# Kernel optimization log

Hardware: AMD Instinct MI355X
Metric: run time of the kernel (lower is better)

Reference implementation:

```python
import jax, jax.numpy as jnp
import numpy as np
from jax import lax

NPOINT = 2048
NSAMPLE = 32
RADIUS = 0.2


def setup_inputs() -> dict:
    key = jax.random.key(0)
    ks = jax.random.split(key, 6)
    B, N, C = 4, 16384, 64
    xyz = jax.random.normal(ks[0], (B, N, 3), jnp.float32)
    features = jax.random.normal(ks[1], (B, C, N), jnp.float32)

    def w(k, o, i):
        return jax.random.normal(k, (o, i), jnp.float32) * (1.0 / np.sqrt(i))

    W1 = w(ks[2], 64, C + 3)
    b1 = jnp.zeros((64,), jnp.float32)
    W2 = w(ks[3], 64, 64)
    b2 = jnp.zeros((64,), jnp.float32)
    W3 = w(ks[4], 128, 64)
    b3 = jnp.zeros((128,), jnp.float32)
    return {"xyz": xyz, "features": features, "W1": W1, "b1": b1,
            "W2": W2, "b2": b2, "W3": W3, "b3": b3}


def _fps(xyz, npoint):
    # Iterative furthest point sampling. xyz: (B, N, 3) -> (B, npoint) int32.
    B, N, _ = xyz.shape

    def step(carry, _):
        dist, last = carry  # dist: (B, N) running min sq-dist to chosen set
        p = jnp.take_along_axis(xyz, last[:, None, None], axis=1)  # (B,1,3)
        d = jnp.sum((xyz - p) ** 2, axis=-1)                        # (B,N)
        dist = jnp.minimum(dist, d)
        nxt = jnp.argmax(dist, axis=-1).astype(jnp.int32)
        return (dist, nxt), nxt

    init = (jnp.full((B, N), 1e10, xyz.dtype), jnp.zeros((B,), jnp.int32))
    _, rest = lax.scan(step, init, None, length=npoint - 1)  # (npoint-1, B)
    idx = jnp.concatenate([jnp.zeros((1, B), jnp.int32), rest], axis=0)
    return idx.T  # (B, npoint)


def _ball_query(xyz, new_xyz):
    # For each centroid pick up to NSAMPLE points within RADIUS (first-found
    # semantics, matching the PointNet++ CUDA ball_query: pad with first hit).
    B, N, _ = xyz.shape
    d2 = jnp.sum((new_xyz[:, :, None, :] - xyz[:, None, :, :]) ** 2, axis=-1)  # (B,S,N)
    cand = jnp.where(d2 < RADIUS * RADIUS, jnp.arange(N, dtype=jnp.int32), N)
    neg_vals, _ = lax.top_k(-cand, NSAMPLE)  # smallest NSAMPLE indices, in order
    sel = -neg_vals                           # (B,S,NSAMPLE)
    first = sel[..., :1]
    sel = jnp.where(sel == N, first, sel)     # pad empties with first hit
    return jnp.where(sel == N, 0, sel)        # fully-empty balls -> index 0


def reference(xyz, features, W1, b1, W2, b2, W3, b3):
    new_xyz_idx = _fps(xyz, NPOINT)                              # (B, S)
    new_xyz = jnp.take_along_axis(xyz, new_xyz_idx[..., None], axis=1)  # (B,S,3)
    idx = _ball_query(xyz, new_xyz)                              # (B,S,ns)
    B, S, ns = idx.shape
    C = features.shape[1]
    # Gather + center neighbor xyz: (B, 3, S, ns)
    gx = jnp.take_along_axis(xyz, idx.reshape(B, S * ns, 1), axis=1)
    gx = gx.reshape(B, S, ns, 3) - new_xyz[:, :, None, :]
    gx = gx.transpose(0, 3, 1, 2)
    # Gather neighbor features: (B, C, S, ns)
    gf = jnp.take_along_axis(features, idx.reshape(B, 1, S * ns), axis=2)
    gf = gf.reshape(B, C, S, ns)
    x = jnp.concatenate([gx, gf], axis=1)  # (B, C+3, S, ns)
    # SharedMLP: 1x1 conv + ReLU stack
    for W, b in ((W1, b1), (W2, b2), (W3, b3)):
        x = jax.nn.relu(jnp.einsum('oi,bisn->bosn', W, x) + b[None, :, None, None])
    new_features = x.max(axis=-1)  # (B, 128, S)
    return new_xyz, new_xyz_idx, new_features, idx
```

## Files before the change

kernel.cpp:

```cpp
#include <hip/hip_runtime.h>
#include <cstdint>

#define BATCH   4
#define NPTS    16384
#define NCH     64
#define NPOINT  2048
#define NSAMP   32
#define NBUCK   (NPTS / 16)

#define OFF_XYZ  0
#define OFF_IDX1 (BATCH*NPOINT*3)
#define OFF_FEAT (OFF_IDX1 + BATCH*NPOINT)
#define OFF_IDX3 (OFF_FEAT + BATCH*128*NPOINT)


__device__ __forceinline__ float sqd_exact(float dx, float dy, float dz) {
    float a = __fmul_rn(dx, dx);
    float b = __fmul_rn(dy, dy);
    float c = __fmul_rn(dz, dz);
    return __fadd_rn(__fadd_rn(a, b), c);
}

__device__ __forceinline__ int part3(int v) {
    return (v & 1) | ((v & 2) << 2) | ((v & 4) << 4) | ((v & 8) << 6);
}

__device__ __forceinline__ unsigned long long wave_max_u64(unsigned hi, unsigned lo) {
#define STAGE(ctrl, rmask)                                                      \
    {                                                                           \
        unsigned ohi = (unsigned)__builtin_amdgcn_update_dpp(0, (int)hi, ctrl, rmask, 0xf, false); \
        unsigned olo = (unsigned)__builtin_amdgcn_update_dpp(0, (int)lo, ctrl, rmask, 0xf, false); \
        bool take = (ohi > hi) || ((ohi == hi) & (olo > lo));                   \
        hi = take ? ohi : hi;                                                   \
        lo = take ? olo : lo;                                                   \
    }
    STAGE(0x111, 0xf)
    STAGE(0x112, 0xf)
    STAGE(0x114, 0xf)
    STAGE(0x118, 0xf)
    STAGE(0x142, 0xa)
    STAGE(0x143, 0xc)
#undef STAGE
    unsigned rhi = (unsigned)__builtin_amdgcn_readlane((int)hi, 63);
    unsigned rlo = (unsigned)__builtin_amdgcn_readlane((int)lo, 63);
    return ((unsigned long long)rhi << 32) | rlo;
}

__global__ __launch_bounds__(1024)
void binsort_kernel(const float* __restrict__ xyz, float* __restrict__ out) {
    const int b = blockIdx.x, t = threadIdx.x, lane = t & 63, wv = t >> 6;
    float4* pts4 = (float4*)(out + OFF_FEAT) + (size_t)b * NPTS;
    const float* xb = xyz + (size_t)b * (NPTS * 3);

    __shared__ int hist[4096];
    __shared__ int wsum[16];
    for (int k = t; k < 4096; k += 1024) hist[k] = 0;
    __syncthreads();

    const int base = t << 4;
    float f[48];
    {
        const float4* v4 = (const float4*)(xb + (size_t)base * 3);
#pragma unroll
        for (int q = 0; q < 12; ++q) {
            float4 v = v4[q];
            f[4*q+0] = v.x; f[4*q+1] = v.y; f[4*q+2] = v.z; f[4*q+3] = v.w;
        }
    }
    int cells[16];
    const float sc = 16.0f / 9.0f;
#pragma unroll
    for (int j = 0; j < 16; ++j) {
        int qx = (int)fminf(fmaxf((f[3*j+0] + 4.5f) * sc, 0.0f), 15.0f);
        int qy = (int)fminf(fmaxf((f[3*j+1] + 4.5f) * sc, 0.0f), 15.0f);
        int qz = (int)fminf(fmaxf((f[3*j+2] + 4.5f) * sc, 0.0f), 15.0f);
        cells[j] = part3(qx) | (part3(qy) << 1) | (part3(qz) << 2);
        atomicAdd(&hist[cells[j]], 1);
    }
    __syncthreads();

    int h0 = hist[4*t], h1 = hist[4*t+1], h2 = hist[4*t+2], h3 = hist[4*t+3];
    int s = h0 + h1 + h2 + h3;
    int ps = s;
#pragma unroll
    for (int off = 1; off <= 32; off <<= 1) {
        int o = __shfl_up(ps, off, 64);
        if (lane >= off) ps += o;
    }
    if (lane == 63) wsum[wv] = ps;
    __syncthreads();
    int wbase = 0;
    for (int w = 0; w < wv; ++w) wbase += wsum[w];
    int excl = wbase + ps - s;
    hist[4*t]   = excl;
    hist[4*t+1] = excl + h0;
    hist[4*t+2] = excl + h0 + h1;
    hist[4*t+3] = excl + h0 + h1 + h2;
    __syncthreads();

#pragma unroll
    for (int j = 0; j < 16; ++j) {
        int pos = atomicAdd(&hist[cells[j]], 1);
        pts4[pos] = make_float4(f[3*j+0], f[3*j+1], f[3*j+2],
                                __int_as_float(base + j));
    }
}

__global__ __launch_bounds__(1024)
void fps_kernel(const float* __restrict__ xyz, float* __restrict__ out) {
    const int b = blockIdx.x, t = threadIdx.x, lane = t & 63;
    const float4* __restrict__ pts = (const float4*)(out + OFF_FEAT) + (size_t)b * NPTS;
    const float* __restrict__ xb = xyz + (size_t)b * (NPTS * 3);
    float* oxyz = out + OFF_XYZ  + (size_t)b * (NPOINT * 3);
    float* oidx = out + OFF_IDX1 + (size_t)b * NPOINT;

    __shared__ float s_dist[NPTS];
    __shared__ unsigned long long s_key[NBUCK];
    __shared__ int s_wl[NBUCK];
    __shared__ int s_cnt;
    __shared__ unsigned long long s_gkey;

    float bnx, bxx, bny, bxy, bnz, bxz;
    {
        float4 p0 = pts[t * 16];
        bnx = bxx = p0.x; bny = bxy = p0.y; bnz = bxz = p0.z;
#pragma unroll
        for (int j = 1; j < 16; ++j) {
            float4 p = pts[t * 16 + j];
            bnx = fminf(bnx, p.x); bxx = fmaxf(bxx, p.x);
            bny = fminf(bny, p.y); bxy = fmaxf(bxy, p.y);
            bnz = fminf(bnz, p.z); bxz = fmaxf(bxz, p.z);
        }
        float4 big = make_float4(1e10f, 1e10f, 1e10f, 1e10f);
#pragma unroll
        for (int k = 0; k < 4; ++k)
            *(float4*)&s_dist[t * 16 + k * 4] = big;
    }
    float maxdG = 1e10f;
    unsigned long long kv = 0;
    if (t == 0) { s_cnt = 0; s_gkey = 0ull; }

    float cx = xb[0], cy = xb[1], cz = xb[2];
    if (t == 0) { oxyz[0] = cx; oxyz[1] = cy; oxyz[2] = cz; oidx[0] = 0.0f; }
    __syncthreads();

    for (int it = 1; it < NPOINT; ++it) {
        float dxl = fmaxf(fmaxf(bnx - cx, cx - bxx), 0.0f);
        float dyl = fmaxf(fmaxf(bny - cy, cy - bxy), 0.0f);
        float dzl = fmaxf(fmaxf(bnz - cz, cz - bxz), 0.0f);
        float bb  = dxl * dxl + dyl * dyl + dzl * dzl;
        bool active = (bb * 0.99999f < maxdG);
        unsigned long long m = __ballot(active);
        int cntw = (int)__popcll(m);
        if (cntw) {
            int basep = 0;
            if (lane == 0) basep = atomicAdd(&s_cnt, cntw);
            basep = __shfl(basep, 0, 64);
            if (active) {
                int pos = basep + (int)__popcll(m & ((1ull << lane) - 1ull));
                s_wl[pos] = t;
            }
        }
        __syncthreads();
        if (t == 0) s_gkey = 0ull;
        const int K = s_cnt;
        const int sub = t & 3;
        for (int w = t >> 2; w < K; w += 256) {
            const int bid = s_wl[w];
            const int p0  = bid * 16 + sub * 4;
            float4 P0 = pts[p0 + 0], P1 = pts[p0 + 1],
                   P2 = pts[p0 + 2], P3 = pts[p0 + 3];
            float4 dv = *(float4*)&s_dist[p0];
            float mv = -1.0f; int bi = 0x7FFFFFFF;
#define UPD(P, DD)                                                              \
            {                                                                   \
                float d  = sqd_exact(__fsub_rn(P.x, cx),                        \
                                     __fsub_rn(P.y, cy),                        \
                                     __fsub_rn(P.z, cz));                       \
                float nd = fminf(DD, d);                                        \
                DD = nd;                                                        \
                int oi = __float_as_int(P.w);                                   \
                bool bet = (nd > mv) || ((nd == mv) & (oi < bi));               \
                mv = bet ? nd : mv;                                             \
                bi = bet ? oi : bi;                                             \
            }
            UPD(P0, dv.x) UPD(P1, dv.y) UPD(P2, dv.z) UPD(P3, dv.w)
#undef UPD
            *(float4*)&s_dist[p0] = dv;
#pragma unroll
            for (int off = 1; off <= 2; off <<= 1) {
                float omv = __shfl_xor(mv, off, 64);
                int   obi = __shfl_xor(bi, off, 64);
                bool take = (omv > mv) || ((omv == mv) & (obi < bi));
                mv = take ? omv : mv;
                bi = take ? obi : bi;
            }
            if (sub == 0)
                s_key[bid] = ((unsigned long long)__float_as_uint(mv) << 32)
                           | (unsigned)((~bi) & 0xFFFF);
        }
        __syncthreads();
        if (active) {
            kv = s_key[t];
            maxdG = __uint_as_float((unsigned)(kv >> 32));
        }
        unsigned long long wk = wave_max_u64((unsigned)(kv >> 32), (unsigned)kv);
        if (lane == 0) atomicMax(&s_gkey, wk);
        if (t == 0) s_cnt = 0;
        __syncthreads();
        unsigned long long gk = s_gkey;
        const int gi = (int)((~(unsigned)gk) & 0xFFFFu);
        cx = xb[gi*3+0]; cy = xb[gi*3+1]; cz = xb[gi*3+2];
        if (t == 0) {
            oxyz[it*3+0] = cx; oxyz[it*3+1] = cy; oxyz[it*3+2] = cz;
            oidx[it] = (float)gi;
        }
    }
}

__global__ __launch_bounds__(256)
void ballq_kernel(const float* __restrict__ xyz, float* __restrict__ out) {
    const int b    = blockIdx.y;
    const int t    = threadIdx.x;
    const int lane = t & 63;
    const int wv   = t >> 6;
    const int s    = blockIdx.x * 4 + wv;
    const float* __restrict__ xb = xyz + (size_t)b * (NPTS * 3);

    const float* ctr = out + OFF_XYZ + ((size_t)(b * NPOINT + s)) * 3;
    const float cx = ctr[0], cy = ctr[1], cz = ctr[2];

    __shared__ float sx[256], sy[256], sz[256];
    __shared__ int   lists[4][NSAMP];

    int have = 0;
    for (int tile = 0; tile < NPTS / 256; ++tile) {
        const int pi = tile * 256 + t;
        const float* p = xb + (size_t)pi * 3;
        float ax = p[0], ay = p[1], az = p[2];
        sx[t] = ax; sy[t] = ay; sz[t] = az;
        __syncthreads();
        if (have < NSAMP) {
#pragma unroll
            for (int sub = 0; sub < 4; ++sub) {
                const int li = sub * 64 + lane;
                float d2 = sqd_exact(__fsub_rn(cx, sx[li]),
                                     __fsub_rn(cy, sy[li]),
                                     __fsub_rn(cz, sz[li]));
                bool hit = d2 < 0.04f;
                unsigned long long m = __ballot(hit);
                if (hit) {
                    int pos = have + (int)__popcll(m & ((1ull << lane) - 1ull));
                    if (pos < NSAMP) lists[wv][pos] = tile * 256 + li;
                }
                have += (int)__popcll(m);
                if (have >= NSAMP) break;
            }
        }
        __syncthreads();
    }
    if (lane < NSAMP) {
        int hv = have < NSAMP ? have : NSAMP;
        int v0 = (have > 0) ? lists[wv][0] : 0;
        int v  = (lane < hv) ? lists[wv][lane] : v0;
        out[OFF_IDX3 + ((size_t)(b * NPOINT + s)) * NSAMP + lane] = (float)v;
    }
}

__global__ __launch_bounds__(256)
void mlp_kernel(const float* __restrict__ xyz, const float* __restrict__ feat,
                const float* __restrict__ W1, const float* __restrict__ b1,
                const float* __restrict__ W2, const float* __restrict__ b2,
                const float* __restrict__ W3, const float* __restrict__ b3,
                float* __restrict__ out) {
    const int s = blockIdx.x;
    const int b = blockIdx.y;
    const int t = threadIdx.x;

    __shared__ __align__(16) float Wbuf[64 * 128];
    __shared__ float Xs[67 * 32];
    __shared__ float H1[64 * 32];
    __shared__ float H2[64 * 32];
    __shared__ int   idxs[NSAMP];
    __shared__ float ctr[3];

    if (t < NSAMP) idxs[t] = (int)out[OFF_IDX3 + ((size_t)(b * NPOINT + s)) * NSAMP + t];
    if (t < 3)     ctr[t]  = out[OFF_XYZ + ((size_t)(b * NPOINT + s)) * 3 + t];
    for (int k = t; k < 67 * 64; k += 256) {
        int i = k >> 6, o = k & 63;
        Wbuf[k] = W1[o * 67 + i];
    }
    __syncthreads();

    const float* xb = xyz  + (size_t)b * (NPTS * 3);
    const float* fb = feat + (size_t)b * (NCH * NPTS);
    for (int k = t; k < 67 * 32; k += 256) {
        int i = k >> 5, n = k & 31;
        int ii = idxs[n];
        float v;
        if (i < 3) v = __fsub_rn(xb[(size_t)ii * 3 + i], ctr[i]);
        else       v = fb[(size_t)(i - 3) * NPTS + ii];
        Xs[k] = v;
    }
    __syncthreads();

    const int n  = t & 31;
    const int og = t >> 5;

    {
        const int o0 = og * 8;
        float acc[8] = {0,0,0,0,0,0,0,0};
        for (int i = 0; i < 67; ++i) {
            float x = Xs[i * 32 + n];
            const float4* wp = (const float4*)&Wbuf[i * 64 + o0];
            float4 w0 = wp[0], w1 = wp[1];
            acc[0] += w0.x * x; acc[1] += w0.y * x; acc[2] += w0.z * x; acc[3] += w0.w * x;
            acc[4] += w1.x * x; acc[5] += w1.y * x; acc[6] += w1.z * x; acc[7] += w1.w * x;
        }
#pragma unroll
        for (int k = 0; k < 8; ++k)
            H1[(o0 + k) * 32 + n] = fmaxf(acc[k] + b1[o0 + k], 0.0f);
    }
    __syncthreads();
    for (int k = t; k < 64 * 64; k += 256) {
        int i = k >> 6, o = k & 63;
        Wbuf[k] = W2[o * 64 + i];
    }
    __syncthreads();

    {
        const int o0 = og * 8;
        float acc[8] = {0,0,0,0,0,0,0,0};
        for (int i = 0; i < 64; ++i) {
            float x = H1[i * 32 + n];
            const float4* wp = (const float4*)&Wbuf[i * 64 + o0];
            float4 w0 = wp[0], w1 = wp[1];
            acc[0] += w0.x * x; acc[1] += w0.y * x; acc[2] += w0.z * x; acc[3] += w0.w * x;
            acc[4] += w1.x * x; acc[5] += w1.y * x; acc[6] += w1.z * x; acc[7] += w1.w * x;
        }
#pragma unroll
        for (int k = 0; k < 8; ++k)
            H2[(o0 + k) * 32 + n] = fmaxf(acc[k] + b2[o0 + k], 0.0f);
    }
    __syncthreads();
    for (int k = t; k < 64 * 128; k += 256) {
        int i = k >> 7, o = k & 127;
        Wbuf[k] = W3[o * 64 + i];
    }
    __syncthreads();

    {
        const int o0 = og * 16;
        float acc[16];
#pragma unroll
        for (int k = 0; k < 16; ++k) acc[k] = 0.0f;
        for (int i = 0; i < 64; ++i) {
            float x = H2[i * 32 + n];
            const float4* wp = (const float4*)&Wbuf[i * 128 + o0];
            float4 w0 = wp[0], w1 = wp[1], w2 = wp[2], w3 = wp[3];
            acc[0]  += w0.x * x; acc[1]  += w0.y * x; acc[2]  += w0.z * x; acc[3]  += w0.w * x;
            acc[4]  += w1.x * x; acc[5]  += w1.y * x; acc[6]  += w1.z * x; acc[7]  += w1.w * x;
            acc[8]  += w2.x * x; acc[9]  += w2.y * x; acc[10] += w2.z * x; acc[11] += w2.w * x;
            acc[12] += w3.x * x; acc[13] += w3.y * x; acc[14] += w3.z * x; acc[15] += w3.w * x;
        }
#pragma unroll
        for (int k = 0; k < 16; ++k) {
            float h = fmaxf(acc[k] + b3[o0 + k], 0.0f);
#pragma unroll
            for (int off = 16; off >= 1; off >>= 1)
                h = fmaxf(h, __shfl_xor(h, off, 64));
            if (n == 0)
                out[OFF_FEAT + (size_t)b * 128 * NPOINT + (size_t)(o0 + k) * NPOINT + s] = h;
        }
    }
}

extern "C" void kernel_launch(void* const* d_in, const int* in_sizes, int n_in,
                              void* d_out, int out_size, void* d_ws, size_t ws_size,
                              hipStream_t stream) {
    const float* xyz  = (const float*)d_in[0];
    const float* feat = (const float*)d_in[1];
    const float* W1   = (const float*)d_in[2];
    const float* b1   = (const float*)d_in[3];
    const float* W2   = (const float*)d_in[4];
    const float* b2   = (const float*)d_in[5];
    const float* W3   = (const float*)d_in[6];
    const float* b3   = (const float*)d_in[7];
    float* out = (float*)d_out;

    binsort_kernel<<<BATCH, 1024, 0, stream>>>(xyz, out);
    fps_kernel<<<BATCH, 1024, 0, stream>>>(xyz, out);
    ballq_kernel<<<dim3(NPOINT / 4, BATCH), 256, 0, stream>>>(xyz, out);
    mlp_kernel<<<dim3(NPOINT, BATCH), 256, 0, stream>>>(xyz, feat, W1, b1, W2, b2, W3, b3, out);
}
```

Before: 3.778 ms.

## Process active FPS buckets wave-locally and cut per-iteration barriers to one

Replaces the block-wide worklist of active buckets (atomic counter, two barriers) with per-wave processing: each wave walks its own ballot mask four buckets at a time, with each 16-lane group handling one bucket and reducing via 16-wide shuffles. The global argmax now goes through double-buffered per-wave keys in shared memory, which leaves one __syncthreads per iteration instead of three. This lowers synchronization overhead in the serial 2047-iteration loop. The trade-off is possible load imbalance, since waves with many active buckets dominate, and lanes sit idle when a wave has fewer than four buckets left.

```diff
diff --git a/kernel.cpp b/kernel.cpp
--- a/kernel.cpp
+++ b/kernel.cpp
@@ -108,7 +108,7 @@
 
 __global__ __launch_bounds__(1024)
 void fps_kernel(const float* __restrict__ xyz, float* __restrict__ out) {
-    const int b = blockIdx.x, t = threadIdx.x, lane = t & 63;
+    const int b = blockIdx.x, t = threadIdx.x, lane = t & 63, wv = t >> 6;
     const float4* __restrict__ pts = (const float4*)(out + OFF_FEAT) + (size_t)b * NPTS;
     const float* __restrict__ xb = xyz + (size_t)b * (NPTS * 3);
     float* oxyz = out + OFF_XYZ  + (size_t)b * (NPOINT * 3);
@@ -116,9 +116,7 @@
 
     __shared__ float s_dist[NPTS];
     __shared__ unsigned long long s_key[NBUCK];
-    __shared__ int s_wl[NBUCK];
-    __shared__ int s_cnt;
-    __shared__ unsigned long long s_gkey;
+    __shared__ unsigned long long s_wkey[2][16];
 
     float bnx, bxx, bny, bxy, bnz, bxz;
     {
@@ -138,78 +136,60 @@
     }
     float maxdG = 1e10f;
     unsigned long long kv = 0;
-    if (t == 0) { s_cnt = 0; s_gkey = 0ull; }
 
     float cx = xb[0], cy = xb[1], cz = xb[2];
     if (t == 0) { oxyz[0] = cx; oxyz[1] = cy; oxyz[2] = cz; oidx[0] = 0.0f; }
     __syncthreads();
 
     for (int it = 1; it < NPOINT; ++it) {
+        const int q = it & 1;
         float dxl = fmaxf(fmaxf(bnx - cx, cx - bxx), 0.0f);
         float dyl = fmaxf(fmaxf(bny - cy, cy - bxy), 0.0f);
         float dzl = fmaxf(fmaxf(bnz - cz, cz - bxz), 0.0f);
         float bb  = dxl * dxl + dyl * dyl + dzl * dzl;
-        bool active = (bb * 0.99999f < maxdG);
+        const bool active = (bb * 0.99999f < maxdG);
         unsigned long long m = __ballot(active);
-        int cntw = (int)__popcll(m);
-        if (cntw) {
-            int basep = 0;
-            if (lane == 0) basep = atomicAdd(&s_cnt, cntw);
-            basep = __shfl(basep, 0, 64);
-            if (active) {
-                int pos = basep + (int)__popcll(m & ((1ull << lane) - 1ull));
-                s_wl[pos] = t;
+        const int g = lane >> 4;
+        while (m) {
+            int b0 = __ffsll(m) - 1;                 m &= m - 1;
+            int b1_ = m ? (__ffsll(m) - 1) : -1; if (m) m &= m - 1;
+            int b2_ = m ? (__ffsll(m) - 1) : -1; if (m) m &= m - 1;
+            int b3_ = m ? (__ffsll(m) - 1) : -1; if (m) m &= m - 1;
+            int lb = (g == 0) ? b0 : ((g == 1) ? b1_ : ((g == 2) ? b2_ : b3_));
+            if (lb >= 0) {
+                const int bid = (wv << 6) + lb;
+                const int pi  = bid * 16 + (lane & 15);
+                float4 P = pts[pi];
+                float d  = sqd_exact(__fsub_rn(P.x, cx),
+                                     __fsub_rn(P.y, cy),
+                                     __fsub_rn(P.z, cz));
+                float nd = fminf(s_dist[pi], d);
+                s_dist[pi] = nd;
+                float mv = nd;
+                int   bi = __float_as_int(P.w);
+#pragma unroll
+                for (int off = 1; off <= 8; off <<= 1) {
+                    float omv = __shfl_xor(mv, off, 16);
+                    int   obi = __shfl_xor(bi, off, 16);
+                    bool take = (omv > mv) || ((omv == mv) & (obi < bi));
+                    mv = take ? omv : mv;
+                    bi = take ? obi : bi;
+                }
+                if ((lane & 15) == 0)
+                    s_key[bid] = ((unsigned long long)__float_as_uint(mv) << 32)
+                               | (unsigned)(~bi);
             }
         }
-        __syncthreads();
-        if (t == 0) s_gkey = 0ull;
-        const int K = s_cnt;
-        const int sub = t & 3;
-        for (int w = t >> 2; w < K; w += 256) {
-            const int bid = s_wl[w];
-            const int p0  = bid * 16 + sub * 4;
-            float4 P0 = pts[p0 + 0], P1 = pts[p0 + 1],
-                   P2 = pts[p0 + 2], P3 = pts[p0 + 3];
-            float4 dv = *(float4*)&s_dist[p0];
-            float mv = -1.0f; int bi = 0x7FFFFFFF;
-#define UPD(P, DD)                                                              \
-            {                                                                   \
-                float d  = sqd_exact(__fsub_rn(P.x, cx),                        \
-                                     __fsub_rn(P.y, cy),                        \
-                                     __fsub_rn(P.z, cz));                       \
-                float nd = fminf(DD, d);                                        \
-                DD = nd;                                                        \
-                int oi = __float_as_int(P.w);                                   \
-                bool bet = (nd > mv) || ((nd == mv) & (oi < bi));               \
-                mv = bet ? nd : mv;                                             \
-                bi = bet ? oi : bi;                                             \
-            }
-            UPD(P0, dv.x) UPD(P1, dv.y) UPD(P2, dv.z) UPD(P3, dv.w)
-#undef UPD
-            *(float4*)&s_dist[p0] = dv;
-#pragma unroll
-            for (int off = 1; off <= 2; off <<= 1) {
-                float omv = __shfl_xor(mv, off, 64);
-                int   obi = __shfl_xor(bi, off, 64);
-                bool take = (omv > mv) || ((omv == mv) & (obi < bi));
-                mv = take ? omv : mv;
-                bi = take ? obi : bi;
-            }
-            if (sub == 0)
-                s_key[bid] = ((unsigned long long)__float_as_uint(mv) << 32)
-                           | (unsigned)((~bi) & 0xFFFF);
-        }
-        __syncthreads();
         if (active) {
             kv = s_key[t];
             maxdG = __uint_as_float((unsigned)(kv >> 32));
         }
         unsigned long long wk = wave_max_u64((unsigned)(kv >> 32), (unsigned)kv);
-        if (lane == 0) atomicMax(&s_gkey, wk);
-        if (t == 0) s_cnt = 0;
+        if (lane == 0) s_wkey[q][wv] = wk;
         __syncthreads();
-        unsigned long long gk = s_gkey;
-        const int gi = (int)((~(unsigned)gk) & 0xFFFFu);
+        unsigned long long kvv = s_wkey[q][lane & 15];
+        unsigned long long gk  = wave_max_u64((unsigned)(kvv >> 32), (unsigned)kvv);
+        const int gi = (int)(~(unsigned)gk);
         cx = xb[gi*3+0]; cy = xb[gi*3+1]; cz = xb[gi*3+2];
         if (t == 0) {
             oxyz[it*3+0] = cx; oxyz[it*3+1] = cy; oxyz[it*3+2] = cz;
```

New measurement: 6.056 ms. +60.3%, slower.
